# Performance work log

Hardware: AMD Instinct MI355X
Metric: run time of the kernel (lower is better)

Reference implementation:

```python
import jax, jax.numpy as jnp
import numpy as np

B_, N, C = 4096, 49, 128
H = 4          # num_heads
NW = 64        # windows per image


def setup_inputs() -> dict:
    key = jax.random.key(0)
    k = jax.random.split(key, 6)
    s = 0.02
    return {
        "x": jax.random.normal(k[0], (B_, N, C), jnp.float32),
        "mask": jax.random.normal(k[1], (NW, N, N), jnp.float32),
        "qkv_w": jax.random.normal(k[2], (3 * C, C), jnp.float32) * s,
        "qkv_b": jax.random.normal(k[3], (3 * C,), jnp.float32) * s,
        "proj_w": jax.random.normal(k[4], (C, C), jnp.float32) * s,
        "proj_b": jax.random.normal(k[5], (C,), jnp.float32) * s,
    }


def reference(x, mask, qkv_w, qkv_b, proj_w, proj_b):
    b, n, c = x.shape
    hd = c // H
    scale = hd ** -0.5
    # fused QKV projection: [b, n, 3, H, hd] -> [3, b, H, n, hd]
    qkv = (x @ qkv_w.T + qkv_b).reshape(b, n, 3, H, hd)
    qkv = jnp.transpose(qkv, (2, 0, 3, 1, 4))
    q, k, v = qkv[0] * scale, qkv[1], qkv[2]
    attn = jnp.einsum("bhnd,bhmd->bhnm", q, k)  # [b, H, n, n]
    nW = mask.shape[0]
    attn = attn.reshape(b // nW, nW, H, n, n) + mask[None, :, None, :, :]
    attn = jax.nn.softmax(attn.reshape(b, H, n, n), axis=-1)
    out = jnp.einsum("bhnm,bhmd->bhnd", attn, v)
    out = jnp.transpose(out, (0, 2, 1, 3)).reshape(b, n, c)
    return out @ proj_w.T + proj_b
```

## Files before the change

### kernel.cpp

```cpp
#include <hip/hip_runtime.h>
#include <hip/hip_bf16.h>

#define C_DIM 128
#define SCALE 0.17677669529663687f

typedef __attribute__((ext_vector_type(8))) short frag8;
typedef __attribute__((ext_vector_type(4))) float f32x4;

#define XACT_STR 136
#define HEAD_SZ  6304
#define KOFF 2000
#define VOFF 4000
#define Q_STR 40
#define VT_STR 72
#define P_STR 72
#define SMEM_TOT 25216

__device__ __forceinline__ unsigned short f2b(float x) {
    __hip_bfloat16 h = __float2bfloat16(x);
    return __builtin_bit_cast(unsigned short, h);
}
__device__ __forceinline__ unsigned pk2(float a, float b) {
    return ((unsigned)f2b(b) << 16) | (unsigned)f2b(a);
}

__global__ void convert_weights(const float4* __restrict__ qkvw,
                                const float4* __restrict__ projw,
                                ushort4* __restrict__ wbf) {
    int i = blockIdx.x * 256 + threadIdx.x;
    float4 v = (i < 12288) ? qkvw[i] : projw[i - 12288];
    ushort4 p;
    p.x = f2b(v.x); p.y = f2b(v.y); p.z = f2b(v.z); p.w = f2b(v.w);
    wbf[i] = p;
}

__global__ __launch_bounds__(256, 3) void attn_mfma(
    const float* __restrict__ x,
    const float* __restrict__ mask,
    const float* __restrict__ qkv_b,
    const float* __restrict__ proj_b,
    const unsigned short* __restrict__ wq,
    float* __restrict__ out)
{
    __shared__ __align__(16) unsigned short sm[SMEM_TOT];

    const int b = blockIdx.x, tid = threadIdx.x;
    const int h    = tid >> 6;
    const int lane = tid & 63;
    const int n16  = lane & 15;
    const int q    = lane >> 4;

    const unsigned short* pw = wq + 49152;
    frag8 wf2[2][4];
#pragma unroll
    for (int ct = 0; ct < 2; ++ct)
#pragma unroll
        for (int ks = 0; ks < 4; ++ks)
            wf2[ct][ks] = *(const frag8*)(pw + (size_t)(h * 32 + ct * 16 + n16) * C_DIM + ks * 32 + q * 8);
    float4 pb4[2];
#pragma unroll
    for (int ct = 0; ct < 2; ++ct)
        pb4[ct] = *(const float4*)(proj_b + h * 32 + ct * 16 + q * 4);

    {
        const float4* xg = (const float4*)(x + (size_t)b * 6272);
        for (int i = tid; i < 1568; i += 256) {
            float4 v = xg[i];
            int row = i >> 5, col = (i & 31) << 2;
            uint2 pk; pk.x = pk2(v.x, v.y); pk.y = pk2(v.z, v.w);
            *(uint2*)&sm[row * XACT_STR + col] = pk;
        }
    }
    __syncthreads();

    frag8 xf[4][4];
#pragma unroll
    for (int tt = 0; tt < 4; ++tt)
#pragma unroll
        for (int ks = 0; ks < 4; ++ks)
            xf[tt][ks] = *(const frag8*)&sm[min(tt * 16 + n16, 48) * XACT_STR + ks * 32 + q * 8];
    __syncthreads();

    const int Hb = h * HEAD_SZ;

#pragma unroll
    for (int mat = 0; mat < 3; ++mat) {
#pragma unroll
        for (int ct = 0; ct < 2; ++ct) {
            const unsigned short* wrow = wq + (size_t)(mat * C_DIM + h * 32 + ct * 16 + n16) * C_DIM;
            frag8 wf[4];
#pragma unroll
            for (int ks = 0; ks < 4; ++ks) wf[ks] = *(const frag8*)(wrow + ks * 32 + q * 8);
            if (mat < 2) {
                float4 b4 = *(const float4*)(qkv_b + mat * C_DIM + h * 32 + ct * 16 + q * 4);
                const float sc = (mat == 0) ? SCALE : 1.f;
                const int base = Hb + ((mat == 0) ? 0 : KOFF);
#pragma unroll
                for (int tt = 0; tt < 4; ++tt) {
                    f32x4 acc = {0.f, 0.f, 0.f, 0.f};
#pragma unroll
                    for (int ks = 0; ks < 4; ++ks)
                        acc = __builtin_amdgcn_mfma_f32_16x16x32_bf16(wf[ks], xf[tt][ks], acc, 0, 0, 0);
                    uint2 pk;
                    pk.x = pk2((acc[0] + b4.x) * sc, (acc[1] + b4.y) * sc);
                    pk.y = pk2((acc[2] + b4.z) * sc, (acc[3] + b4.w) * sc);
                    *(uint2*)&sm[base + min(tt * 16 + n16, 49) * Q_STR + ct * 16 + q * 4] = pk;
                }
            } else {
                float bias = qkv_b[2 * C_DIM + h * 32 + ct * 16 + n16];
#pragma unroll
                for (int tt = 0; tt < 4; ++tt) {
                    f32x4 acc = {0.f, 0.f, 0.f, 0.f};
#pragma unroll
                    for (int ks = 0; ks < 4; ++ks)
                        acc = __builtin_amdgcn_mfma_f32_16x16x32_bf16(xf[tt][ks], wf[ks], acc, 0, 0, 0);
                    uint2 pk;
                    pk.x = pk2(acc[0] + bias, acc[1] + bias);
                    pk.y = pk2(acc[2] + bias, acc[3] + bias);
                    *(uint2*)&sm[Hb + VOFF + (ct * 16 + n16) * VT_STR + tt * 16 + q * 4] = pk;
                }
            }
        }
    }

    frag8 qf[4], kf[4];
#pragma unroll
    for (int t = 0; t < 4; ++t) {
        qf[t] = *(const frag8*)&sm[Hb + (t * 16 + n16) * Q_STR + q * 8];
        kf[t] = *(const frag8*)&sm[Hb + KOFF + (t * 16 + n16) * Q_STR + q * 8];
    }
    const float* mrow = mask + (size_t)(b & 63) * 2401;
    f32x4 s[4][4];
#pragma unroll
    for (int it = 0; it < 4; ++it) {
        int ii = min(it * 16 + n16, 48);
#pragma unroll
        for (int jt = 0; jt < 3; ++jt) {
            const float* mp = mrow + ii * 49 + jt * 16 + q * 4;
            s[jt][it] = (f32x4){mp[0], mp[1], mp[2], mp[3]};
        }
        float m48 = (q == 0) ? mrow[ii * 49 + 48] : 0.f;
        s[3][it] = (f32x4){m48, 0.f, 0.f, 0.f};
    }
#pragma unroll
    for (int jt = 0; jt < 4; ++jt)
#pragma unroll
        for (int it = 0; it < 4; ++it)
            s[jt][it] = __builtin_amdgcn_mfma_f32_16x16x32_bf16(kf[jt], qf[it], s[jt][it], 0, 0, 0);

#pragma unroll
    for (int it = 0; it < 4; ++it) {
        float mx = -1e30f;
#pragma unroll
        for (int jt = 0; jt < 4; ++jt)
#pragma unroll
            for (int r = 0; r < 4; ++r)
                if (jt * 16 + q * 4 + r < 49) mx = fmaxf(mx, s[jt][it][r]);
        mx = fmaxf(mx, __shfl_xor(mx, 16));
        mx = fmaxf(mx, __shfl_xor(mx, 32));
        float sum = 0.f;
#pragma unroll
        for (int jt = 0; jt < 4; ++jt)
#pragma unroll
            for (int r = 0; r < 4; ++r) {
                float e = (jt * 16 + q * 4 + r < 49) ? __expf(s[jt][it][r] - mx) : 0.f;
                s[jt][it][r] = e;
                sum += e;
            }
        sum += __shfl_xor(sum, 16);
        sum += __shfl_xor(sum, 32);
        float inv = __builtin_amdgcn_rcpf(sum);
#pragma unroll
        for (int jt = 0; jt < 4; ++jt) {
            uint2 pk;
            pk.x = pk2(s[jt][it][0] * inv, s[jt][it][1] * inv);
            pk.y = pk2(s[jt][it][2] * inv, s[jt][it][3] * inv);
            *(uint2*)&sm[Hb + min(it * 16 + n16, 49) * P_STR + jt * 16 + q * 4] = pk;
        }
    }

    frag8 vf[2][2];
#pragma unroll
    for (int ct = 0; ct < 2; ++ct)
#pragma unroll
        for (int ks = 0; ks < 2; ++ks)
            vf[ct][ks] = *(const frag8*)&sm[Hb + VOFF + (ct * 16 + n16) * VT_STR + ks * 32 + q * 8];
    f32x4 o[2][4];
#pragma unroll
    for (int ct = 0; ct < 2; ++ct)
#pragma unroll
        for (int nt = 0; nt < 4; ++nt) o[ct][nt] = (f32x4){0.f, 0.f, 0.f, 0.f};
#pragma unroll
    for (int nt = 0; nt < 4; ++nt)
#pragma unroll
        for (int ks = 0; ks < 2; ++ks) {
            frag8 pf = *(const frag8*)&sm[Hb + min(nt * 16 + n16, 49) * P_STR + ks * 32 + q * 8];
#pragma unroll
            for (int ct = 0; ct < 2; ++ct)
                o[ct][nt] = __builtin_amdgcn_mfma_f32_16x16x32_bf16(vf[ct][ks], pf, o[ct][nt], 0, 0, 0);
        }
    __syncthreads();

#pragma unroll
    for (int ct = 0; ct < 2; ++ct)
#pragma unroll
        for (int nt = 0; nt < 4; ++nt) {
            uint2 pk;
            pk.x = pk2(o[ct][nt][0], o[ct][nt][1]);
            pk.y = pk2(o[ct][nt][2], o[ct][nt][3]);
            *(uint2*)&sm[min(nt * 16 + n16, 49) * XACT_STR + h * 32 + ct * 16 + q * 4] = pk;
        }
    __syncthreads();

    float* outb = out + (size_t)b * 6272;
#pragma unroll
    for (int nt = 0; nt < 4; ++nt) {
        frag8 af[4];
#pragma unroll
        for (int ks = 0; ks < 4; ++ks)
            af[ks] = *(const frag8*)&sm[min(nt * 16 + n16, 48) * XACT_STR + ks * 32 + q * 8];
        int tok = nt * 16 + n16;
#pragma unroll
        for (int ct = 0; ct < 2; ++ct) {
            f32x4 acc = {0.f, 0.f, 0.f, 0.f};
#pragma unroll
            for (int ks = 0; ks < 4; ++ks)
                acc = __builtin_amdgcn_mfma_f32_16x16x32_bf16(wf2[ct][ks], af[ks], acc, 0, 0, 0);
            if (tok < 49)
                *(float4*)&outb[tok * C_DIM + h * 32 + ct * 16 + q * 4] =
                    make_float4(acc[0] + pb4[ct].x, acc[1] + pb4[ct].y,
                                acc[2] + pb4[ct].z, acc[3] + pb4[ct].w);
        }
    }
}

extern "C" void kernel_launch(void* const* d_in, const int* in_sizes, int n_in,
                              void* d_out, int out_size, void* d_ws, size_t ws_size,
                              hipStream_t stream) {
    const float* x      = (const float*)d_in[0];
    const float* mask   = (const float*)d_in[1];
    const float* qkv_b  = (const float*)d_in[3];
    const float* proj_b = (const float*)d_in[5];

    unsigned short* wbf = (unsigned short*)d_ws;
    convert_weights<<<64, 256, 0, stream>>>((const float4*)d_in[2],
                                            (const float4*)d_in[4],
                                            (ushort4*)wbf);
    attn_mfma<<<4096, 256, 0, stream>>>(x, mask, qkv_b, proj_b, wbf, (float*)d_out);
}
```

Measured before the change: 268.4 us.

## Pre-pad mask to 64-wide rows and vectorize mask loads; batch LDS fragment loads

Adds a pad_mask kernel that rewrites the 64x49x49 mask into a zero-padded 64x49x64 float buffer in workspace, so the attention kernel can read each mask row with aligned float4 loads instead of scalar loads. The mask is now added after the QK MFMAs rather than used as the accumulator init. The max/sum reductions in softmax use tree form, QKV biases are hoisted to registers at kernel start, and the P and attention-output fragments are loaded from LDS in batches ahead of the MFMAs. This costs an extra kernel launch and more live registers, which could reduce occupancy under the 3-blocks-per-CU bound.

```diff
diff --git a/kernel.cpp b/kernel.cpp
--- a/kernel.cpp
+++ b/kernel.cpp
@@ -23,6 +23,9 @@
 __device__ __forceinline__ unsigned pk2(float a, float b) {
     return ((unsigned)f2b(b) << 16) | (unsigned)f2b(a);
 }
+__device__ __forceinline__ void add4(f32x4& a, float4 m) {
+    a[0] += m.x; a[1] += m.y; a[2] += m.z; a[3] += m.w;
+}
 
 __global__ void convert_weights(const float4* __restrict__ qkvw,
                                 const float4* __restrict__ projw,
@@ -34,9 +37,22 @@
     wbf[i] = p;
 }
 
+__global__ void pad_mask(const float* __restrict__ mask, float* __restrict__ pm) {
+    int t = blockIdx.x * 256 + threadIdx.x;
+    int w = t / 784, rem = t % 784, i = rem >> 4, tq = rem & 15;
+    const float* src = mask + (size_t)w * 2401 + i * 49;
+    int j = tq * 4;
+    float4 v;
+    v.x = (j     < 49) ? src[j]     : 0.f;
+    v.y = (j + 1 < 49) ? src[j + 1] : 0.f;
+    v.z = (j + 2 < 49) ? src[j + 2] : 0.f;
+    v.w = (j + 3 < 49) ? src[j + 3] : 0.f;
+    ((float4*)pm)[t] = v;
+}
+
 __global__ __launch_bounds__(256, 3) void attn_mfma(
     const float* __restrict__ x,
-    const float* __restrict__ mask,
+    const float* __restrict__ pmask,
     const float* __restrict__ qkv_b,
     const float* __restrict__ proj_b,
     const unsigned short* __restrict__ wq,
@@ -58,9 +74,16 @@
         for (int ks = 0; ks < 4; ++ks)
             wf2[ct][ks] = *(const frag8*)(pw + (size_t)(h * 32 + ct * 16 + n16) * C_DIM + ks * 32 + q * 8);
     float4 pb4[2];
-#pragma unroll
-    for (int ct = 0; ct < 2; ++ct)
+    float4 b4m[2][2];
+    float  bV[2];
+#pragma unroll
+    for (int ct = 0; ct < 2; ++ct) {
         pb4[ct] = *(const float4*)(proj_b + h * 32 + ct * 16 + q * 4);
+#pragma unroll
+        for (int mat = 0; mat < 2; ++mat)
+            b4m[mat][ct] = *(const float4*)(qkv_b + mat * C_DIM + h * 32 + ct * 16 + q * 4);
+        bV[ct] = qkv_b[2 * C_DIM + h * 32 + ct * 16 + n16];
+    }
 
     {
         const float4* xg = (const float4*)(x + (size_t)b * 6272);
@@ -92,7 +115,7 @@
 #pragma unroll
             for (int ks = 0; ks < 4; ++ks) wf[ks] = *(const frag8*)(wrow + ks * 32 + q * 8);
             if (mat < 2) {
-                float4 b4 = *(const float4*)(qkv_b + mat * C_DIM + h * 32 + ct * 16 + q * 4);
+                float4 b4 = b4m[mat][ct];
                 const float sc = (mat == 0) ? SCALE : 1.f;
                 const int base = Hb + ((mat == 0) ? 0 : KOFF);
 #pragma unroll
@@ -107,7 +130,7 @@
                     *(uint2*)&sm[base + min(tt * 16 + n16, 49) * Q_STR + ct * 16 + q * 4] = pk;
                 }
             } else {
-                float bias = qkv_b[2 * C_DIM + h * 32 + ct * 16 + n16];
+                float bias = bV[ct];
 #pragma unroll
                 for (int tt = 0; tt < 4; ++tt) {
                     f32x4 acc = {0.f, 0.f, 0.f, 0.f};
@@ -129,44 +152,60 @@
         qf[t] = *(const frag8*)&sm[Hb + (t * 16 + n16) * Q_STR + q * 8];
         kf[t] = *(const frag8*)&sm[Hb + KOFF + (t * 16 + n16) * Q_STR + q * 8];
     }
-    const float* mrow = mask + (size_t)(b & 63) * 2401;
     f32x4 s[4][4];
+#pragma unroll
+    for (int jt = 0; jt < 4; ++jt)
+#pragma unroll
+        for (int it = 0; it < 4; ++it)
+            s[jt][it] = (f32x4){0.f, 0.f, 0.f, 0.f};
+#pragma unroll
+    for (int jt = 0; jt < 4; ++jt)
+#pragma unroll
+        for (int it = 0; it < 4; ++it)
+            s[jt][it] = __builtin_amdgcn_mfma_f32_16x16x32_bf16(kf[jt], qf[it], s[jt][it], 0, 0, 0);
+
+    const float* pmrow = pmask + (size_t)(b & 63) * 3136;
 #pragma unroll
     for (int it = 0; it < 4; ++it) {
         int ii = min(it * 16 + n16, 48);
-#pragma unroll
-        for (int jt = 0; jt < 3; ++jt) {
-            const float* mp = mrow + ii * 49 + jt * 16 + q * 4;
-            s[jt][it] = (f32x4){mp[0], mp[1], mp[2], mp[3]};
-        }
-        float m48 = (q == 0) ? mrow[ii * 49 + 48] : 0.f;
-        s[3][it] = (f32x4){m48, 0.f, 0.f, 0.f};
-    }
-#pragma unroll
-    for (int jt = 0; jt < 4; ++jt)
-#pragma unroll
-        for (int it = 0; it < 4; ++it)
-            s[jt][it] = __builtin_amdgcn_mfma_f32_16x16x32_bf16(kf[jt], qf[it], s[jt][it], 0, 0, 0);
-
-#pragma unroll
-    for (int it = 0; it < 4; ++it) {
-        float mx = -1e30f;
+        const float* mp = pmrow + ii * 64 + q * 4;
+        float4 m0 = *(const float4*)(mp);
+        float4 m1 = *(const float4*)(mp + 16);
+        float4 m2 = *(const float4*)(mp + 32);
+        float4 m3 = *(const float4*)(mp + 48);
+        add4(s[0][it], m0); add4(s[1][it], m1);
+        add4(s[2][it], m2); add4(s[3][it], m3);
+
+        float val[16];
 #pragma unroll
         for (int jt = 0; jt < 4; ++jt)
 #pragma unroll
             for (int r = 0; r < 4; ++r)
-                if (jt * 16 + q * 4 + r < 49) mx = fmaxf(mx, s[jt][it][r]);
+                val[jt * 4 + r] = (jt * 16 + q * 4 + r < 49) ? s[jt][it][r] : -1e30f;
+#pragma unroll
+        for (int st = 8; st >= 1; st >>= 1)
+#pragma unroll
+            for (int k = 0; k < 8; ++k)
+                if (k < st) val[k] = fmaxf(val[k], val[k + st]);
+        float mx = val[0];
         mx = fmaxf(mx, __shfl_xor(mx, 16));
         mx = fmaxf(mx, __shfl_xor(mx, 32));
-        float sum = 0.f;
+
+        float ev[16];
 #pragma unroll
         for (int jt = 0; jt < 4; ++jt)
 #pragma unroll
             for (int r = 0; r < 4; ++r) {
                 float e = (jt * 16 + q * 4 + r < 49) ? __expf(s[jt][it][r] - mx) : 0.f;
                 s[jt][it][r] = e;
-                sum += e;
+                ev[jt * 4 + r] = e;
             }
+#pragma unroll
+        for (int st = 8; st >= 1; st >>= 1)
+#pragma unroll
+            for (int k = 0; k < 8; ++k)
+                if (k < st) ev[k] += ev[k + st];
+        float sum = ev[0];
         sum += __shfl_xor(sum, 16);
         sum += __shfl_xor(sum, 32);
         float inv = __builtin_amdgcn_rcpf(sum);
@@ -185,6 +224,12 @@
 #pragma unroll
         for (int ks = 0; ks < 2; ++ks)
             vf[ct][ks] = *(const frag8*)&sm[Hb + VOFF + (ct * 16 + n16) * VT_STR + ks * 32 + q * 8];
+    frag8 pfa[4][2];
+#pragma unroll
+    for (int nt = 0; nt < 4; ++nt)
+#pragma unroll
+        for (int ks = 0; ks < 2; ++ks)
+            pfa[nt][ks] = *(const frag8*)&sm[Hb + min(nt * 16 + n16, 49) * P_STR + ks * 32 + q * 8];
     f32x4 o[2][4];
 #pragma unroll
     for (int ct = 0; ct < 2; ++ct)
@@ -193,12 +238,10 @@
 #pragma unroll
     for (int nt = 0; nt < 4; ++nt)
 #pragma unroll
-        for (int ks = 0; ks < 2; ++ks) {
-            frag8 pf = *(const frag8*)&sm[Hb + min(nt * 16 + n16, 49) * P_STR + ks * 32 + q * 8];
+        for (int ks = 0; ks < 2; ++ks)
 #pragma unroll
             for (int ct = 0; ct < 2; ++ct)
-                o[ct][nt] = __builtin_amdgcn_mfma_f32_16x16x32_bf16(vf[ct][ks], pf, o[ct][nt], 0, 0, 0);
-        }
+                o[ct][nt] = __builtin_amdgcn_mfma_f32_16x16x32_bf16(vf[ct][ks], pfa[nt][ks], o[ct][nt], 0, 0, 0);
     __syncthreads();
 
 #pragma unroll
@@ -213,19 +256,21 @@
     __syncthreads();
 
     float* outb = out + (size_t)b * 6272;
+    frag8 af[4][4];
+#pragma unroll
+    for (int nt = 0; nt < 4; ++nt)
+#pragma unroll
+        for (int ks = 0; ks < 4; ++ks)
+            af[nt][ks] = *(const frag8*)&sm[min(nt * 16 + n16, 48) * XACT_STR + ks * 32 + q * 8];
 #pragma unroll
     for (int nt = 0; nt < 4; ++nt) {
-        frag8 af[4];
-#pragma unroll
-        for (int ks = 0; ks < 4; ++ks)
-            af[ks] = *(const frag8*)&sm[min(nt * 16 + n16, 48) * XACT_STR + ks * 32 + q * 8];
         int tok = nt * 16 + n16;
 #pragma unroll
         for (int ct = 0; ct < 2; ++ct) {
             f32x4 acc = {0.f, 0.f, 0.f, 0.f};
 #pragma unroll
             for (int ks = 0; ks < 4; ++ks)
-                acc = __builtin_amdgcn_mfma_f32_16x16x32_bf16(wf2[ct][ks], af[ks], acc, 0, 0, 0);
+                acc = __builtin_amdgcn_mfma_f32_16x16x32_bf16(wf2[ct][ks], af[nt][ks], acc, 0, 0, 0);
             if (tok < 49)
                 *(float4*)&outb[tok * C_DIM + h * 32 + ct * 16 + q * 4] =
                     make_float4(acc[0] + pb4[ct].x, acc[1] + pb4[ct].y,
@@ -243,8 +288,10 @@
     const float* proj_b = (const float*)d_in[5];
 
     unsigned short* wbf = (unsigned short*)d_ws;
+    float* pmask = (float*)((char*)d_ws + 131072);
     convert_weights<<<64, 256, 0, stream>>>((const float4*)d_in[2],
                                             (const float4*)d_in[4],
                                             (ushort4*)wbf);
-    attn_mfma<<<4096, 256, 0, stream>>>(x, mask, qkv_b, proj_b, wbf, (float*)d_out);
-}
+    pad_mask<<<196, 256, 0, stream>>>(mask, pmask);
+    attn_mfma<<<4096, 256, 0, stream>>>(x, pmask, qkv_b, proj_b, wbf, (float*)d_out);
+}
```

New measurement: 278.6 us. 3.8% more time.

## Keep Q and P in registers via lane shuffles, pad mask, raise occupancy

Applied to the files above, without the earlier changes.

Q is no longer staged through shared memory. Lane shuffles rebuild Q and the softmax probabilities into MFMA B-operand fragments, and the attention loop runs row-tile by row-tile with the 1/sum normalisation deferred to the output accumulator. A small prologue kernel pads the mask to 64-column float4 rows so mask loads are vectorised and aligned. Shared memory drops and launch bounds rise to 4 blocks per CU, with projection-weight loads moved later to shorten register lifetimes. In exchange it adds shuffle instructions, an extra kernel launch and a risk of register spills at the higher occupancy target.

```diff
diff --git a/kernel.cpp b/kernel.cpp
--- a/kernel.cpp
+++ b/kernel.cpp
@@ -6,15 +6,14 @@
 
 typedef __attribute__((ext_vector_type(8))) short frag8;
 typedef __attribute__((ext_vector_type(4))) float f32x4;
+typedef __attribute__((ext_vector_type(4))) unsigned int u32x4;
 
 #define XACT_STR 136
-#define HEAD_SZ  6304
-#define KOFF 2000
-#define VOFF 4000
+#define VT_BASE 8000
+#define VT_PER_HEAD 2304
 #define Q_STR 40
 #define VT_STR 72
-#define P_STR 72
-#define SMEM_TOT 25216
+#define SMEM_TOT 17216
 
 __device__ __forceinline__ unsigned short f2b(float x) {
     __hip_bfloat16 h = __float2bfloat16(x);
@@ -22,6 +21,9 @@
 }
 __device__ __forceinline__ unsigned pk2(float a, float b) {
     return ((unsigned)f2b(b) << 16) | (unsigned)f2b(a);
+}
+__device__ __forceinline__ void add4(f32x4& a, float4 m) {
+    a[0] += m.x; a[1] += m.y; a[2] += m.z; a[3] += m.w;
 }
 
 __global__ void convert_weights(const float4* __restrict__ qkvw,
@@ -34,9 +36,22 @@
     wbf[i] = p;
 }
 
-__global__ __launch_bounds__(256, 3) void attn_mfma(
+__global__ void pad_mask(const float* __restrict__ mask, float* __restrict__ pm) {
+    int t = blockIdx.x * 256 + threadIdx.x;
+    int w = t / 784, rem = t % 784, i = rem >> 4, tq = rem & 15;
+    const float* src = mask + (size_t)w * 2401 + i * 49;
+    int j = tq * 4;
+    float4 v;
+    v.x = (j     < 49) ? src[j]     : 0.f;
+    v.y = (j + 1 < 49) ? src[j + 1] : 0.f;
+    v.z = (j + 2 < 49) ? src[j + 2] : 0.f;
+    v.w = (j + 3 < 49) ? src[j + 3] : 0.f;
+    ((float4*)pm)[t] = v;
+}
+
+__global__ __launch_bounds__(256, 4) void attn_mfma(
     const float* __restrict__ x,
-    const float* __restrict__ mask,
+    const float* __restrict__ pmask,
     const float* __restrict__ qkv_b,
     const float* __restrict__ proj_b,
     const unsigned short* __restrict__ wq,
@@ -49,18 +64,6 @@
     const int lane = tid & 63;
     const int n16  = lane & 15;
     const int q    = lane >> 4;
-
-    const unsigned short* pw = wq + 49152;
-    frag8 wf2[2][4];
-#pragma unroll
-    for (int ct = 0; ct < 2; ++ct)
-#pragma unroll
-        for (int ks = 0; ks < 4; ++ks)
-            wf2[ct][ks] = *(const frag8*)(pw + (size_t)(h * 32 + ct * 16 + n16) * C_DIM + ks * 32 + q * 8);
-    float4 pb4[2];
-#pragma unroll
-    for (int ct = 0; ct < 2; ++ct)
-        pb4[ct] = *(const float4*)(proj_b + h * 32 + ct * 16 + q * 4);
 
     {
         const float4* xg = (const float4*)(x + (size_t)b * 6272);
@@ -81,125 +84,176 @@
             xf[tt][ks] = *(const frag8*)&sm[min(tt * 16 + n16, 48) * XACT_STR + ks * 32 + q * 8];
     __syncthreads();
 
-    const int Hb = h * HEAD_SZ;
-
-#pragma unroll
-    for (int mat = 0; mat < 3; ++mat) {
-#pragma unroll
-        for (int ct = 0; ct < 2; ++ct) {
-            const unsigned short* wrow = wq + (size_t)(mat * C_DIM + h * 32 + ct * 16 + n16) * C_DIM;
-            frag8 wf[4];
-#pragma unroll
-            for (int ks = 0; ks < 4; ++ks) wf[ks] = *(const frag8*)(wrow + ks * 32 + q * 8);
-            if (mat < 2) {
-                float4 b4 = *(const float4*)(qkv_b + mat * C_DIM + h * 32 + ct * 16 + q * 4);
-                const float sc = (mat == 0) ? SCALE : 1.f;
-                const int base = Hb + ((mat == 0) ? 0 : KOFF);
-#pragma unroll
-                for (int tt = 0; tt < 4; ++tt) {
-                    f32x4 acc = {0.f, 0.f, 0.f, 0.f};
-#pragma unroll
-                    for (int ks = 0; ks < 4; ++ks)
-                        acc = __builtin_amdgcn_mfma_f32_16x16x32_bf16(wf[ks], xf[tt][ks], acc, 0, 0, 0);
-                    uint2 pk;
-                    pk.x = pk2((acc[0] + b4.x) * sc, (acc[1] + b4.y) * sc);
-                    pk.y = pk2((acc[2] + b4.z) * sc, (acc[3] + b4.w) * sc);
-                    *(uint2*)&sm[base + min(tt * 16 + n16, 49) * Q_STR + ct * 16 + q * 4] = pk;
-                }
-            } else {
-                float bias = qkv_b[2 * C_DIM + h * 32 + ct * 16 + n16];
-#pragma unroll
-                for (int tt = 0; tt < 4; ++tt) {
-                    f32x4 acc = {0.f, 0.f, 0.f, 0.f};
-#pragma unroll
-                    for (int ks = 0; ks < 4; ++ks)
-                        acc = __builtin_amdgcn_mfma_f32_16x16x32_bf16(xf[tt][ks], wf[ks], acc, 0, 0, 0);
-                    uint2 pk;
-                    pk.x = pk2(acc[0] + bias, acc[1] + bias);
-                    pk.y = pk2(acc[2] + bias, acc[3] + bias);
-                    *(uint2*)&sm[Hb + VOFF + (ct * 16 + n16) * VT_STR + tt * 16 + q * 4] = pk;
-                }
-            }
-        }
-    }
-
-    frag8 qf[4], kf[4];
-#pragma unroll
-    for (int t = 0; t < 4; ++t) {
-        qf[t] = *(const frag8*)&sm[Hb + (t * 16 + n16) * Q_STR + q * 8];
-        kf[t] = *(const frag8*)&sm[Hb + KOFF + (t * 16 + n16) * Q_STR + q * 8];
-    }
-    const float* mrow = mask + (size_t)(b & 63) * 2401;
-    f32x4 s[4][4];
+    const int KB = h * 2000;
+    const int VB = VT_BASE + h * VT_PER_HEAD;
+
+#pragma unroll
+    for (int ct = 0; ct < 2; ++ct) {
+        const unsigned short* wrow = wq + (size_t)(C_DIM + h * 32 + ct * 16 + n16) * C_DIM;
+        frag8 wf[4];
+#pragma unroll
+        for (int ks = 0; ks < 4; ++ks) wf[ks] = *(const frag8*)(wrow + ks * 32 + q * 8);
+        float4 b4 = *(const float4*)(qkv_b + C_DIM + h * 32 + ct * 16 + q * 4);
+#pragma unroll
+        for (int tt = 0; tt < 4; ++tt) {
+            f32x4 acc = {0.f, 0.f, 0.f, 0.f};
+#pragma unroll
+            for (int ks = 0; ks < 4; ++ks)
+                acc = __builtin_amdgcn_mfma_f32_16x16x32_bf16(wf[ks], xf[tt][ks], acc, 0, 0, 0);
+            uint2 pk;
+            pk.x = pk2(acc[0] + b4.x, acc[1] + b4.y);
+            pk.y = pk2(acc[2] + b4.z, acc[3] + b4.w);
+            *(uint2*)&sm[KB + min(tt * 16 + n16, 49) * Q_STR + ct * 16 + q * 4] = pk;
+        }
+    }
+#pragma unroll
+    for (int ct = 0; ct < 2; ++ct) {
+        const unsigned short* wrow = wq + (size_t)(2 * C_DIM + h * 32 + ct * 16 + n16) * C_DIM;
+        frag8 wf[4];
+#pragma unroll
+        for (int ks = 0; ks < 4; ++ks) wf[ks] = *(const frag8*)(wrow + ks * 32 + q * 8);
+        float bias = qkv_b[2 * C_DIM + h * 32 + ct * 16 + n16];
+#pragma unroll
+        for (int tt = 0; tt < 4; ++tt) {
+            f32x4 acc = {0.f, 0.f, 0.f, 0.f};
+#pragma unroll
+            for (int ks = 0; ks < 4; ++ks)
+                acc = __builtin_amdgcn_mfma_f32_16x16x32_bf16(xf[tt][ks], wf[ks], acc, 0, 0, 0);
+            uint2 pk;
+            pk.x = pk2(acc[0] + bias, acc[1] + bias);
+            pk.y = pk2(acc[2] + bias, acc[3] + bias);
+            *(uint2*)&sm[VB + (ct * 16 + n16) * VT_STR + tt * 16 + q * 4] = pk;
+        }
+    }
+    unsigned qw[4][2][2];
+#pragma unroll
+    for (int ct = 0; ct < 2; ++ct) {
+        const unsigned short* wrow = wq + (size_t)(h * 32 + ct * 16 + n16) * C_DIM;
+        frag8 wf[4];
+#pragma unroll
+        for (int ks = 0; ks < 4; ++ks) wf[ks] = *(const frag8*)(wrow + ks * 32 + q * 8);
+        float4 b4 = *(const float4*)(qkv_b + h * 32 + ct * 16 + q * 4);
+#pragma unroll
+        for (int tt = 0; tt < 4; ++tt) {
+            f32x4 acc = {0.f, 0.f, 0.f, 0.f};
+#pragma unroll
+            for (int ks = 0; ks < 4; ++ks)
+                acc = __builtin_amdgcn_mfma_f32_16x16x32_bf16(wf[ks], xf[tt][ks], acc, 0, 0, 0);
+            qw[tt][ct][0] = pk2((acc[0] + b4.x) * SCALE, (acc[1] + b4.y) * SCALE);
+            qw[tt][ct][1] = pk2((acc[2] + b4.z) * SCALE, (acc[3] + b4.w) * SCALE);
+        }
+    }
+
+    const int srcA = ((q & 1) << 5) + n16;
+    const int srcB = srcA + 16;
+    const int hi = q >> 1;
+    frag8 qf[4];
+#pragma unroll
+    for (int it = 0; it < 4; ++it) {
+        unsigned a00 = __shfl((int)qw[it][0][0], srcA);
+        unsigned a10 = __shfl((int)qw[it][1][0], srcA);
+        unsigned a01 = __shfl((int)qw[it][0][1], srcA);
+        unsigned a11 = __shfl((int)qw[it][1][1], srcA);
+        unsigned b00 = __shfl((int)qw[it][0][0], srcB);
+        unsigned b10 = __shfl((int)qw[it][1][0], srcB);
+        unsigned b01 = __shfl((int)qw[it][0][1], srcB);
+        unsigned b11 = __shfl((int)qw[it][1][1], srcB);
+        u32x4 t;
+        t[0] = hi ? a10 : a00;
+        t[1] = hi ? a11 : a01;
+        t[2] = hi ? b10 : b00;
+        t[3] = hi ? b11 : b01;
+        qf[it] = __builtin_bit_cast(frag8, t);
+    }
+
+    frag8 kf[4];
+#pragma unroll
+    for (int t = 0; t < 4; ++t)
+        kf[t] = *(const frag8*)&sm[KB + (t * 16 + n16) * Q_STR + q * 8];
+    frag8 vf[2][2];
+#pragma unroll
+    for (int ct = 0; ct < 2; ++ct)
+#pragma unroll
+        for (int ks = 0; ks < 2; ++ks)
+            vf[ct][ks] = *(const frag8*)&sm[VB + (ct * 16 + n16) * VT_STR + ks * 32 + q * 8];
+    __syncthreads();
+
+    const float4* pm4 = (const float4*)(pmask + (size_t)(b & 63) * 3136);
+    f32x4 o[2][4];
+#pragma unroll
+    for (int ct = 0; ct < 2; ++ct)
+#pragma unroll
+        for (int nt = 0; nt < 4; ++nt) o[ct][nt] = (f32x4){0.f, 0.f, 0.f, 0.f};
+
 #pragma unroll
     for (int it = 0; it < 4; ++it) {
         int ii = min(it * 16 + n16, 48);
-#pragma unroll
-        for (int jt = 0; jt < 3; ++jt) {
-            const float* mp = mrow + ii * 49 + jt * 16 + q * 4;
-            s[jt][it] = (f32x4){mp[0], mp[1], mp[2], mp[3]};
-        }
-        float m48 = (q == 0) ? mrow[ii * 49 + 48] : 0.f;
-        s[3][it] = (f32x4){m48, 0.f, 0.f, 0.f};
-    }
-#pragma unroll
-    for (int jt = 0; jt < 4; ++jt)
-#pragma unroll
-        for (int it = 0; it < 4; ++it)
-            s[jt][it] = __builtin_amdgcn_mfma_f32_16x16x32_bf16(kf[jt], qf[it], s[jt][it], 0, 0, 0);
-
-#pragma unroll
-    for (int it = 0; it < 4; ++it) {
+        float4 mj[4];
+#pragma unroll
+        for (int jt = 0; jt < 4; ++jt) mj[jt] = pm4[ii * 16 + q + jt * 4];
+
+        f32x4 s4[4];
+#pragma unroll
+        for (int jt = 0; jt < 4; ++jt) {
+            s4[jt] = (f32x4){0.f, 0.f, 0.f, 0.f};
+            s4[jt] = __builtin_amdgcn_mfma_f32_16x16x32_bf16(kf[jt], qf[it], s4[jt], 0, 0, 0);
+        }
+#pragma unroll
+        for (int jt = 0; jt < 4; ++jt) add4(s4[jt], mj[jt]);
+
         float mx = -1e30f;
 #pragma unroll
         for (int jt = 0; jt < 4; ++jt)
 #pragma unroll
             for (int r = 0; r < 4; ++r)
-                if (jt * 16 + q * 4 + r < 49) mx = fmaxf(mx, s[jt][it][r]);
+                if (jt * 16 + q * 4 + r < 49) mx = fmaxf(mx, s4[jt][r]);
         mx = fmaxf(mx, __shfl_xor(mx, 16));
         mx = fmaxf(mx, __shfl_xor(mx, 32));
+
         float sum = 0.f;
 #pragma unroll
         for (int jt = 0; jt < 4; ++jt)
 #pragma unroll
             for (int r = 0; r < 4; ++r) {
-                float e = (jt * 16 + q * 4 + r < 49) ? __expf(s[jt][it][r] - mx) : 0.f;
-                s[jt][it][r] = e;
+                float e = (jt * 16 + q * 4 + r < 49) ? __expf(s4[jt][r] - mx) : 0.f;
+                s4[jt][r] = e;
                 sum += e;
             }
         sum += __shfl_xor(sum, 16);
         sum += __shfl_xor(sum, 32);
         float inv = __builtin_amdgcn_rcpf(sum);
+
+        unsigned pw[4][2];
 #pragma unroll
         for (int jt = 0; jt < 4; ++jt) {
-            uint2 pk;
-            pk.x = pk2(s[jt][it][0] * inv, s[jt][it][1] * inv);
-            pk.y = pk2(s[jt][it][2] * inv, s[jt][it][3] * inv);
-            *(uint2*)&sm[Hb + min(it * 16 + n16, 49) * P_STR + jt * 16 + q * 4] = pk;
-        }
-    }
-
-    frag8 vf[2][2];
-#pragma unroll
-    for (int ct = 0; ct < 2; ++ct)
-#pragma unroll
-        for (int ks = 0; ks < 2; ++ks)
-            vf[ct][ks] = *(const frag8*)&sm[Hb + VOFF + (ct * 16 + n16) * VT_STR + ks * 32 + q * 8];
-    f32x4 o[2][4];
-#pragma unroll
-    for (int ct = 0; ct < 2; ++ct)
-#pragma unroll
-        for (int nt = 0; nt < 4; ++nt) o[ct][nt] = (f32x4){0.f, 0.f, 0.f, 0.f};
-#pragma unroll
-    for (int nt = 0; nt < 4; ++nt)
+            pw[jt][0] = pk2(s4[jt][0], s4[jt][1]);
+            pw[jt][1] = pk2(s4[jt][2], s4[jt][3]);
+        }
 #pragma unroll
         for (int ks = 0; ks < 2; ++ks) {
-            frag8 pf = *(const frag8*)&sm[Hb + min(nt * 16 + n16, 49) * P_STR + ks * 32 + q * 8];
+            unsigned a0  = __shfl((int)pw[2 * ks][0],     srcA);
+            unsigned a0h = __shfl((int)pw[2 * ks + 1][0], srcA);
+            unsigned a1  = __shfl((int)pw[2 * ks][1],     srcA);
+            unsigned a1h = __shfl((int)pw[2 * ks + 1][1], srcA);
+            unsigned b0  = __shfl((int)pw[2 * ks][0],     srcB);
+            unsigned b0h = __shfl((int)pw[2 * ks + 1][0], srcB);
+            unsigned b1  = __shfl((int)pw[2 * ks][1],     srcB);
+            unsigned b1h = __shfl((int)pw[2 * ks + 1][1], srcB);
+            u32x4 t;
+            t[0] = hi ? a0h : a0;
+            t[1] = hi ? a1h : a1;
+            t[2] = hi ? b0h : b0;
+            t[3] = hi ? b1h : b1;
+            frag8 pf = __builtin_bit_cast(frag8, t);
 #pragma unroll
             for (int ct = 0; ct < 2; ++ct)
-                o[ct][nt] = __builtin_amdgcn_mfma_f32_16x16x32_bf16(vf[ct][ks], pf, o[ct][nt], 0, 0, 0);
-        }
-    __syncthreads();
+                o[ct][it] = __builtin_amdgcn_mfma_f32_16x16x32_bf16(vf[ct][ks], pf, o[ct][it], 0, 0, 0);
+        }
+#pragma unroll
+        for (int ct = 0; ct < 2; ++ct)
+#pragma unroll
+            for (int r = 0; r < 4; ++r) o[ct][it][r] *= inv;
+    }
 
 #pragma unroll
     for (int ct = 0; ct < 2; ++ct)
@@ -210,22 +264,36 @@
             pk.y = pk2(o[ct][nt][2], o[ct][nt][3]);
             *(uint2*)&sm[min(nt * 16 + n16, 49) * XACT_STR + h * 32 + ct * 16 + q * 4] = pk;
         }
+
+    const unsigned short* pwq = wq + 49152;
+    frag8 wf2[2][4];
+#pragma unroll
+    for (int ct = 0; ct < 2; ++ct)
+#pragma unroll
+        for (int ks = 0; ks < 4; ++ks)
+            wf2[ct][ks] = *(const frag8*)(pwq + (size_t)(h * 32 + ct * 16 + n16) * C_DIM + ks * 32 + q * 8);
+    float4 pb4[2];
+#pragma unroll
+    for (int ct = 0; ct < 2; ++ct)
+        pb4[ct] = *(const float4*)(proj_b + h * 32 + ct * 16 + q * 4);
     __syncthreads();
 
     float* outb = out + (size_t)b * 6272;
+    frag8 af[4][4];
+#pragma unroll
+    for (int nt = 0; nt < 4; ++nt)
+#pragma unroll
+        for (int ks = 0; ks < 4; ++ks)
+            af[nt][ks] = *(const frag8*)&sm[min(nt * 16 + n16, 48) * XACT_STR + ks * 32 + q * 8];
 #pragma unroll
     for (int nt = 0; nt < 4; ++nt) {
-        frag8 af[4];
-#pragma unroll
-        for (int ks = 0; ks < 4; ++ks)
-            af[ks] = *(const frag8*)&sm[min(nt * 16 + n16, 48) * XACT_STR + ks * 32 + q * 8];
         int tok = nt * 16 + n16;
 #pragma unroll
         for (int ct = 0; ct < 2; ++ct) {
             f32x4 acc = {0.f, 0.f, 0.f, 0.f};
 #pragma unroll
             for (int ks = 0; ks < 4; ++ks)
-                acc = __builtin_amdgcn_mfma_f32_16x16x32_bf16(wf2[ct][ks], af[ks], acc, 0, 0, 0);
+                acc = __builtin_amdgcn_mfma_f32_16x16x32_bf16(wf2[ct][ks], af[nt][ks], acc, 0, 0, 0);
             if (tok < 49)
                 *(float4*)&outb[tok * C_DIM + h * 32 + ct * 16 + q * 4] =
                     make_float4(acc[0] + pb4[ct].x, acc[1] + pb4[ct].y,
@@ -243,8 +311,10 @@
     const float* proj_b = (const float*)d_in[5];
 
     unsigned short* wbf = (unsigned short*)d_ws;
+    float* pmask = (float*)((char*)d_ws + 131072);
     convert_weights<<<64, 256, 0, stream>>>((const float4*)d_in[2],
                                             (const float4*)d_in[4],
                                             (ushort4*)wbf);
-    attn_mfma<<<4096, 256, 0, stream>>>(x, mask, qkv_b, proj_b, wbf, (float*)d_out);
-}
+    pad_mask<<<196, 256, 0, stream>>>(mask, pmask);
+    attn_mfma<<<4096, 256, 0, stream>>>(x, pmask, qkv_b, proj_b, wbf, (float*)d_out);
+}
```

New measurement: 326.7 us. 21.7% more time.
